# Kernel tuning notes

Hardware: AMD Instinct MI355X
Metric: run time of the kernel (lower is better)

## Reference

```python
import jax, jax.numpy as jnp
import numpy as np

WS = 11
SIGMA = 1.5
L = 1.0  # val_range


def _gaussian_window(ws=WS, sigma=SIGMA):
    x = np.arange(ws, dtype=np.float64) - ws // 2
    g = np.exp(-(x ** 2) / (2.0 * sigma ** 2))
    g = g / g.sum()
    w2d = np.outer(g, g)
    return jnp.asarray(w2d, dtype=jnp.float32)  # [ws, ws]


def _depthwise_blur(x, w2d):
    # x: [B, C, H, W]; depthwise gaussian conv with SAME-style padding ws//2
    c = x.shape[1]
    kern = jnp.broadcast_to(w2d, (c, 1, WS, WS)).astype(x.dtype)  # OIHW, groups=C
    pad = WS // 2
    return jax.lax.conv_general_dilated(
        x, kern, window_strides=(1, 1), padding=[(pad, pad), (pad, pad)],
        dimension_numbers=('NCHW', 'OIHW', 'NCHW'), feature_group_count=c)


def setup_inputs() -> dict:
    key = jax.random.key(0)
    k1, k2 = jax.random.split(key)
    img1 = jax.random.uniform(k1, (32, 3, 512, 512), dtype=jnp.float32)
    img2 = jax.random.uniform(k2, (32, 3, 512, 512), dtype=jnp.float32)
    return {"img1": img1, "img2": img2}


def reference(img1, img2):
    w2d = _gaussian_window()
    mu1 = _depthwise_blur(img1, w2d)
    mu2 = _depthwise_blur(img2, w2d)
    mu1_sq = mu1 * mu1
    mu2_sq = mu2 * mu2
    mu1_mu2 = mu1 * mu2
    sigma1_sq = _depthwise_blur(img1 * img1, w2d) - mu1_sq
    sigma2_sq = _depthwise_blur(img2 * img2, w2d) - mu2_sq
    sigma12 = _depthwise_blur(img1 * img2, w2d) - mu1_mu2
    C1 = (0.01 * L) ** 2
    C2 = (0.03 * L) ** 2
    ssim_map = ((2.0 * mu1_mu2 + C1) * (2.0 * sigma12 + C2)) / (
        (mu1_sq + mu2_sq + C1) * (sigma1_sq + sigma2_sq + C2))
    return 1.0 - ssim_map.mean()
```

## Files before the change

kernel.cpp:

```cpp
#include <hip/hip_runtime.h>
#include <math.h>

typedef _Float16 f16;
typedef _Float16 f16x2 __attribute__((ext_vector_type(2)));
typedef _Float16 f16x8 __attribute__((ext_vector_type(8)));
typedef _Float16 f16x4 __attribute__((ext_vector_type(4)));
typedef float f32x4 __attribute__((ext_vector_type(4)));

#define ROWS 88
#define NTHREADS 256

__device__ __forceinline__ float ssim_px(float m1, float m2, float mss, float m12) {
  const float C1 = 0.0001f, C2 = 0.0009f;
  const float mu1s = m1 * m1, mu2s = m2 * m2, mu12 = m1 * m2;
  const float num = (2.f * mu12 + C1) * (2.f * (m12 - mu12) + C2);
  const float den = (mu1s + mu2s + C1) * (mss - mu1s - mu2s + C2);
  return num * __builtin_amdgcn_rcpf(den);
}

__device__ __forceinline__ unsigned pk2(float a, float b) {
  return __builtin_bit_cast(unsigned, __builtin_amdgcn_cvt_pkrtz(a, b));
}

#define H_ISSUE(RG, S)                                                         \
  {                                                                            \
    const int rimg = gy0 + (RG) * 16 + n;                                      \
    size_t base;                                                               \
    if (MASKED) {                                                              \
      const bool octok = (xb >= 0) && (xb <= 504);                             \
      const bool rok = (rimg >= 0) && (rimg < 512);                            \
      ok[S] = (rok && octok) ? 1.f : 0.f;                                      \
      base = ((size_t)(rok ? rimg : 0) << 9) + (size_t)(octok ? xb : 0);       \
    } else {                                                                   \
      ok[S] = 1.f;                                                             \
      base = ((size_t)rimg << 9) + (size_t)xb;                                 \
    }                                                                          \
    A0[S] = *(const float4*)(p1 + base);                                       \
    A1[S] = *(const float4*)(p1 + base + 4);                                   \
    B0[S] = *(const float4*)(p2 + base);                                       \
    B1[S] = *(const float4*)(p2 + base + 4);                                   \
  }

#define H_CONSUME(RG, S)                                                       \
  {                                                                            \
    float4 a0 = A0[S], a1 = A1[S], b0 = B0[S], b1 = B1[S];                     \
    if (MASKED) {                                                              \
      const float m = ok[S];                                                   \
      a0.x *= m; a0.y *= m; a0.z *= m; a0.w *= m;                              \
      a1.x *= m; a1.y *= m; a1.z *= m; a1.w *= m;                              \
      b0.x *= m; b0.y *= m; b0.z *= m; b0.w *= m;                              \
      b1.x *= m; b1.y *= m; b1.z *= m; b1.w *= m;                              \
    }                                                                          \
    union { f16x8 v; unsigned u[4]; } ua, ub;                                  \
    ua.u[0] = pk2(a0.x, a0.y); ua.u[1] = pk2(a0.z, a0.w);                      \
    ua.u[2] = pk2(a1.x, a1.y); ua.u[3] = pk2(a1.z, a1.w);                      \
    ub.u[0] = pk2(b0.x, b0.y); ub.u[1] = pk2(b0.z, b0.w);                      \
    ub.u[2] = pk2(b1.x, b1.y); ub.u[3] = pk2(b1.z, b1.w);                      \
    const f16x8 fa = ua.v, fb = ub.v;                                          \
    const f16x8 fp = fa * fb;                                \
    const f16x8 fs = fa * fa + fb * fb;               \
    const f32x4 z = {0.f, 0.f, 0.f, 0.f};                                      \
    const f32x4 Da = __builtin_amdgcn_mfma_f32_16x16x32_f16(fa, Bh, z, 0, 0, 0); \
    const f32x4 Db = __builtin_amdgcn_mfma_f32_16x16x32_f16(fb, Bh, z, 0, 0, 0); \
    const f32x4 Ds = __builtin_amdgcn_mfma_f32_16x16x32_f16(fs, Bh, z, 0, 0, 0); \
    const f32x4 Dp = __builtin_amdgcn_mfma_f32_16x16x32_f16(fp, Bh, z, 0, 0, 0); \
    const int sr = (RG) * 16 + kg * 4;                                         \
    const f16x4 wa = {(f16)Da[0], (f16)Da[1], (f16)Da[2], (f16)Da[3]};         \
    const f16x4 wb = {(f16)Db[0], (f16)Db[1], (f16)Db[2], (f16)Db[3]};         \
    const f16x4 ws = {(f16)Ds[0], (f16)Ds[1], (f16)Ds[2], (f16)Ds[3]};         \
    const f16x4 wp = {(f16)Dp[0], (f16)Dp[1], (f16)Dp[2], (f16)Dp[3]};         \
    *(f16x4*)&si[0][px][sr] = wa;                                              \
    *(f16x4*)&si[1][px][sr] = wb;                                              \
    *(f16x4*)&si[2][px][sr] = ws;                                              \
    *(f16x4*)&si[3][px][sr] = wp;                                              \
  }

template <bool MASKED>
__device__ __forceinline__ void h_phase(
    const float* __restrict__ p1, const float* __restrict__ p2,
    f16 (*si)[64][ROWS],
    int gy0, int xb, int px, int n, int kg, const f16x8& Bh)
{
  float4 A0[2], A1[2], B0[2], B1[2];
  float ok[2];
  H_ISSUE(0, 0)
  H_ISSUE(1, 1)
  __builtin_amdgcn_sched_barrier(0);
  H_CONSUME(0, 0)
  H_ISSUE(2, 0)
  __builtin_amdgcn_sched_barrier(0);
  H_CONSUME(1, 1)
  H_ISSUE(3, 1)
  __builtin_amdgcn_sched_barrier(0);
  H_CONSUME(2, 0)
  H_ISSUE(4, 0)
  __builtin_amdgcn_sched_barrier(0);
  H_CONSUME(3, 1)
  H_CONSUME(4, 0)
}

__global__ __launch_bounds__(NTHREADS) void ssim_main_kernel(
    const float* __restrict__ img1, const float* __restrict__ img2,
    float* __restrict__ partials, float norm, float cexp)
{
  __shared__ f16 si[4][64][ROWS];
  __shared__ float sred[4];

  const int tid = threadIdx.x;
  const int wv = tid >> 6, lane = tid & 63;
  const int n = lane & 15, kg = lane >> 4;

  int b = blockIdx.x;
  const int tx = b & 7; b >>= 3;
  const int ty = b & 7; b >>= 3;
  const float* __restrict__ p1 = img1 + (size_t)b * 262144;
  const float* __restrict__ p2 = img2 + (size_t)b * 262144;

  f16x8 Bh, Av;
#pragma unroll
  for (int i = 0; i < 8; i++) {
    const int k = 8 * kg + i;
    {
      const int idx = k - n - 3;
      const float d = (float)(idx - 5);
      const float val = norm * exp2f(cexp * d * d);
      Bh[i] = (idx >= 0 && idx <= 10) ? (f16)val : (f16)0.f;
    }
    {
      const int idx = k - n;
      const float d = (float)(idx - 5);
      const float val = norm * exp2f(cexp * d * d);
      Av[i] = (idx >= 0 && idx <= 10) ? (f16)val : (f16)0.f;
    }
  }

  const int X0 = tx * 64 + wv * 16;
  const int xb = X0 - 8 + 8 * kg;
  const int gy0 = ty * 64 - 5;
  const int px = wv * 16 + n;

  const bool interior = (tx >= 1) && (tx <= 6) && (ty >= 1) && (ty <= 6);
  if (interior)
    h_phase<false>(p1, p2, si, gy0, xb, px, n, kg, Bh);
  else
    h_phase<true>(p1, p2, si, gy0, xb, px, n, kg, Bh);

  float acc4[4] = {0.f, 0.f, 0.f, 0.f};
#pragma unroll
  for (int og = 0; og < 4; og++) {
    const int srb = og * 16 + 8 * kg;
    const f16x8 Ba = *(const f16x8*)&si[0][px][srb];
    const f16x8 Bb = *(const f16x8*)&si[1][px][srb];
    const f16x8 Bs = *(const f16x8*)&si[2][px][srb];
    const f16x8 Bp = *(const f16x8*)&si[3][px][srb];
    const f32x4 z = {0.f, 0.f, 0.f, 0.f};
    const f32x4 Ma = __builtin_amdgcn_mfma_f32_16x16x32_f16(Av, Ba, z, 0, 0, 0);
    const f32x4 Mb = __builtin_amdgcn_mfma_f32_16x16x32_f16(Av, Bb, z, 0, 0, 0);
    const f32x4 Ms = __builtin_amdgcn_mfma_f32_16x16x32_f16(Av, Bs, z, 0, 0, 0);
    const f32x4 Mp = __builtin_amdgcn_mfma_f32_16x16x32_f16(Av, Bp, z, 0, 0, 0);
#pragma unroll
    for (int r = 0; r < 4; r++)
      acc4[r] += ssim_px(Ma[r], Mb[r], Ms[r], Mp[r]);
  }
  float accSum = (acc4[0] + acc4[1]) + (acc4[2] + acc4[3]);

  for (int off = 32; off > 0; off >>= 1)
    accSum += __shfl_down(accSum, off, 64);
  if (lane == 0) sred[wv] = accSum;
  __syncthreads();
  if (tid == 0)
    partials[blockIdx.x] = sred[0] + sred[1] + sred[2] + sred[3];
}

__global__ __launch_bounds__(256) void ssim_final_kernel(
    const float* __restrict__ partials, float* __restrict__ out,
    int n, double invN)
{
  __shared__ double sred[4];
  const int tid = threadIdx.x;
  double s = 0.0;
  for (int i = tid; i < n; i += 256) s += (double)partials[i];
  for (int off = 32; off > 0; off >>= 1)
    s += __shfl_down(s, off, 64);
  if ((tid & 63) == 0) sred[tid >> 6] = s;
  __syncthreads();
  if (tid == 0) {
    double tot = 0.0;
#pragma unroll
    for (int i = 0; i < 4; i++) tot += sred[i];
    out[0] = (float)(1.0 - tot * invN);
  }
}

extern "C" void kernel_launch(void* const* d_in, const int* in_sizes, int n_in,
                              void* d_out, int out_size, void* d_ws, size_t ws_size,
                              hipStream_t stream) {
  const float* img1 = (const float*)d_in[0];
  const float* img2 = (const float*)d_in[1];
  float* out = (float*)d_out;
  float* partials = (float*)d_ws;

  const int planes = in_sizes[0] / (512 * 512);
  const int nBlocks = planes * 8 * 8;

  double sum = 0.0;
  for (int i = 0; i < 11; i++) {
    const double x = (double)(i - 5);
    sum += exp(-(x * x) / 4.5);
  }
  const float norm = (float)(1.0 / sum);
  const float cexp = (float)(-1.0 / (4.5 * 0.6931471805599453));

  const double invN = 1.0 / (double)in_sizes[0];

  ssim_main_kernel<<<nBlocks, NTHREADS, 0, stream>>>(img1, img2, partials, norm, cexp);
  ssim_final_kernel<<<1, 256, 0, stream>>>(partials, out, nBlocks, invN);
}
```

Measured before the change: 73.33 us.

## Fuse final reduction into main kernel via last-block atomic counter

Removes the separate final-reduction kernel launch: each block writes its partial, increments a global atomic counter, and the last block to finish sums all partials and writes the result. A memset of the counter is added before the launch. The f32-to-f16 conversions of the MFMA outputs now use packed round-toward-zero converts instead of per-element casts. The change trades one kernel launch for a memset plus a tail serial reduction in one block, and rounding mode changes slightly.

```diff
diff --git a/kernel.cpp b/kernel.cpp
--- a/kernel.cpp
+++ b/kernel.cpp
@@ -2,7 +2,6 @@
 #include <math.h>
 
 typedef _Float16 f16;
-typedef _Float16 f16x2 __attribute__((ext_vector_type(2)));
 typedef _Float16 f16x8 __attribute__((ext_vector_type(8)));
 typedef _Float16 f16x4 __attribute__((ext_vector_type(4)));
 typedef float f32x4 __attribute__((ext_vector_type(4)));
@@ -20,6 +19,12 @@
 
 __device__ __forceinline__ unsigned pk2(float a, float b) {
   return __builtin_bit_cast(unsigned, __builtin_amdgcn_cvt_pkrtz(a, b));
+}
+__device__ __forceinline__ f16x4 pk4(const f32x4& d) {
+  union { unsigned u[2]; f16x4 v; } r;
+  r.u[0] = pk2(d[0], d[1]);
+  r.u[1] = pk2(d[2], d[3]);
+  return r.v;
 }
 
 #define H_ISSUE(RG, S)                                                         \
@@ -65,14 +70,10 @@
     const f32x4 Ds = __builtin_amdgcn_mfma_f32_16x16x32_f16(fs, Bh, z, 0, 0, 0); \
     const f32x4 Dp = __builtin_amdgcn_mfma_f32_16x16x32_f16(fp, Bh, z, 0, 0, 0); \
     const int sr = (RG) * 16 + kg * 4;                                         \
-    const f16x4 wa = {(f16)Da[0], (f16)Da[1], (f16)Da[2], (f16)Da[3]};         \
-    const f16x4 wb = {(f16)Db[0], (f16)Db[1], (f16)Db[2], (f16)Db[3]};         \
-    const f16x4 ws = {(f16)Ds[0], (f16)Ds[1], (f16)Ds[2], (f16)Ds[3]};         \
-    const f16x4 wp = {(f16)Dp[0], (f16)Dp[1], (f16)Dp[2], (f16)Dp[3]};         \
-    *(f16x4*)&si[0][px][sr] = wa;                                              \
-    *(f16x4*)&si[1][px][sr] = wb;                                              \
-    *(f16x4*)&si[2][px][sr] = ws;                                              \
-    *(f16x4*)&si[3][px][sr] = wp;                                              \
+    *(f16x4*)&si[0][px][sr] = pk4(Da);                                         \
+    *(f16x4*)&si[1][px][sr] = pk4(Db);                                         \
+    *(f16x4*)&si[2][px][sr] = pk4(Ds);                                         \
+    *(f16x4*)&si[3][px][sr] = pk4(Dp);                                         \
   }
 
 template <bool MASKED>
@@ -101,10 +102,12 @@
 
 __global__ __launch_bounds__(NTHREADS) void ssim_main_kernel(
     const float* __restrict__ img1, const float* __restrict__ img2,
-    float* __restrict__ partials, float norm, float cexp)
+    unsigned* __restrict__ counter, float* __restrict__ partials,
+    float* __restrict__ out, float norm, float cexp, double invN, int nBlocks)
 {
   __shared__ f16 si[4][64][ROWS];
   __shared__ float sred[4];
+  __shared__ bool lastBlock;
 
   const int tid = threadIdx.x;
   const int wv = tid >> 6, lane = tid & 63;
@@ -168,27 +171,25 @@
     accSum += __shfl_down(accSum, off, 64);
   if (lane == 0) sred[wv] = accSum;
   __syncthreads();
-  if (tid == 0)
+  if (tid == 0) {
     partials[blockIdx.x] = sred[0] + sred[1] + sred[2] + sred[3];
-}
-
-__global__ __launch_bounds__(256) void ssim_final_kernel(
-    const float* __restrict__ partials, float* __restrict__ out,
-    int n, double invN)
-{
-  __shared__ double sred[4];
-  const int tid = threadIdx.x;
-  double s = 0.0;
-  for (int i = tid; i < n; i += 256) s += (double)partials[i];
-  for (int off = 32; off > 0; off >>= 1)
-    s += __shfl_down(s, off, 64);
-  if ((tid & 63) == 0) sred[tid >> 6] = s;
+    __threadfence();
+    const unsigned old = atomicAdd(counter, 1u);
+    lastBlock = (old == (unsigned)nBlocks - 1u);
+  }
   __syncthreads();
-  if (tid == 0) {
-    double tot = 0.0;
-#pragma unroll
-    for (int i = 0; i < 4; i++) tot += sred[i];
-    out[0] = (float)(1.0 - tot * invN);
+
+  if (lastBlock) {
+    __threadfence();
+    double s = 0.0;
+    for (int i = tid; i < nBlocks; i += NTHREADS) s += (double)partials[i];
+    for (int off = 32; off > 0; off >>= 1)
+      s += __shfl_down(s, off, 64);
+    __shared__ double dred[4];
+    if (lane == 0) dred[wv] = s;
+    __syncthreads();
+    if (tid == 0)
+      out[0] = (float)(1.0 - (dred[0] + dred[1] + dred[2] + dred[3]) * invN);
   }
 }
 
@@ -198,7 +199,8 @@
   const float* img1 = (const float*)d_in[0];
   const float* img2 = (const float*)d_in[1];
   float* out = (float*)d_out;
-  float* partials = (float*)d_ws;
+  unsigned* counter = (unsigned*)d_ws;
+  float* partials = (float*)((char*)d_ws + 256);
 
   const int planes = in_sizes[0] / (512 * 512);
   const int nBlocks = planes * 8 * 8;
@@ -213,6 +215,7 @@
 
   const double invN = 1.0 / (double)in_sizes[0];
 
-  ssim_main_kernel<<<nBlocks, NTHREADS, 0, stream>>>(img1, img2, partials, norm, cexp);
-  ssim_final_kernel<<<1, 256, 0, stream>>>(partials, out, nBlocks, invN);
-}
+  hipMemsetAsync(d_ws, 0, 4, stream);
+  ssim_main_kernel<<<nBlocks, NTHREADS, 0, stream>>>(
+      img1, img2, counter, partials, out, norm, cexp, invN, nBlocks);
+}
```

New measurement: 274.4 us. 274% more time.
